# Optimization experiments

Hardware: AMD Instinct MI355X
Metric: run time of the kernel (lower is better)

## Reference

```python
import jax, jax.numpy as jnp
import numpy as np

N, IN_F, OUT_F = 8192, 4096, 4096
QMIN, QMAX = -128, 127  # int8 range for bitwidth 8


def setup_inputs() -> dict:
    key = jax.random.key(0)
    k1, k2, k3, k4 = jax.random.split(key, 4)
    x = jax.random.randint(k1, (N, IN_F), QMIN, QMAX + 1, dtype=jnp.int32).astype(jnp.int8)
    weight = jax.random.randint(k2, (OUT_F, IN_F), QMIN, QMAX + 1, dtype=jnp.int32).astype(jnp.int8)
    bias = jax.random.randint(k3, (OUT_F,), -1024, 1024, dtype=jnp.int32)
    weight_scale = jax.random.uniform(k4, (OUT_F,), dtype=jnp.float32, minval=0.001, maxval=0.02)
    input_scale = jnp.asarray([0.05], dtype=jnp.float32)
    output_scale = jnp.asarray([0.1], dtype=jnp.float32)
    output_zero_point = 0
    return {"x": x, "weight": weight, "bias": bias, "weight_scale": weight_scale,
            "input_scale": input_scale, "output_scale": output_scale,
            "output_zero_point": output_zero_point}


def reference(x, weight, bias, weight_scale, input_scale, output_scale, output_zero_point):
    # int32-accumulated GEMM with bias (CPU path of the torch module)
    acc = jnp.matmul(x.astype(jnp.int32), weight.astype(jnp.int32).T) + bias[None, :]  # [N, OUT_F] int32
    # fused dequant/requant epilogue
    scale_factor = (input_scale * weight_scale / output_scale)[None, :]  # [1, OUT_F]
    out = acc.astype(jnp.float32) * scale_factor + output_zero_point
    out = jnp.clip(jnp.round(out), QMIN, QMAX).astype(jnp.int8)
    return out
```

## Files before the change

### kernel.cpp

```cpp
#include <hip/hip_runtime.h>
#include <stdint.h>


#define M_DIM 8192
#define N_DIM 4096
#define K_DIM 4096
#define BM 128
#define BN 128
#define BK 64

using i32x4 = __attribute__((ext_vector_type(4))) int;

typedef const __attribute__((address_space(1))) uint32_t* gptr_t;
typedef __attribute__((address_space(3))) uint32_t* lptr_t;

__device__ __forceinline__ void gload_lds16(const void* g, void* l) {
    __builtin_amdgcn_global_load_lds((gptr_t)g, (lptr_t)l, 16, 0, 0);
}

__device__ __forceinline__ int pack4(i32x4 v) {
    return (int)(((unsigned)v.x & 0xFFu) | (((unsigned)v.y & 0xFFu) << 8) |
                 (((unsigned)v.z & 0xFFu) << 16) | (((unsigned)v.w) << 24));
}

__global__ void pack_i8_kernel(const int* __restrict__ src, int8_t* __restrict__ dst, int n_elems) {
    int idx = blockIdx.x * blockDim.x + threadIdx.x;
    int stride = gridDim.x * blockDim.x;
    int n16 = n_elems >> 4;
    for (int i = idx; i < n16; i += stride) {
        const i32x4* s = (const i32x4*)(src + (size_t)i * 16);
        i32x4 v0 = s[0], v1 = s[1], v2 = s[2], v3 = s[3];
        i32x4 o;
        o.x = pack4(v0); o.y = pack4(v1); o.z = pack4(v2); o.w = pack4(v3);
        *(i32x4*)(dst + (size_t)i * 16) = o;
    }
}

template<bool PACKED>
__global__ void qgemm_kernel(const void* __restrict__ xp, const void* __restrict__ wp,
                             const int* __restrict__ bias, const float* __restrict__ wscale,
                             const float* __restrict__ iscale, const float* __restrict__ oscale,
                             const int* __restrict__ zp, int* __restrict__ out) {
    __shared__ int8_t As[BM][BK];
    __shared__ int8_t Bs[BN][BK];

    const int tid  = threadIdx.x;
    const int wave = tid >> 6;
    const int lane = tid & 63;

    int b = blockIdx.x;
    int s = (b & 7) * (gridDim.x >> 3) + (b >> 3);
    const int bcol = (s & 31) * BN;
    const int brow = (s >> 5) * BM;

    const int wr = wave >> 1;
    const int wc = wave & 1;

    i32x4 acc[4][4] = {};

    for (int kt = 0; kt < K_DIM; kt += BK) {
        if constexpr (PACKED) {
            const int8_t* x8 = (const int8_t*)xp;
            const int8_t* w8 = (const int8_t*)wp;
            #pragma unroll
            for (int i = 0; i < 2; i++) {
                int c = wave * 2 + i;
                int row = c * 16 + (lane >> 2);
                int colb = (lane & 3) * 16;
                gload_lds16(x8 + (size_t)(brow + row) * K_DIM + kt + colb, &As[c * 16][0]);
                gload_lds16(w8 + (size_t)(bcol + row) * K_DIM + kt + colb, &Bs[c * 16][0]);
            }
        } else {
            const int* x32 = (const int*)xp;
            const int* w32 = (const int*)wp;
            int row = tid >> 1;
            int h = tid & 1;
            const i32x4* sa = (const i32x4*)(x32 + (size_t)(brow + row) * K_DIM + kt + h * 32);
            const i32x4* sb = (const i32x4*)(w32 + (size_t)(bcol + row) * K_DIM + kt + h * 32);
            int pa[8], pb[8];
            #pragma unroll
            for (int j = 0; j < 8; j++) { pa[j] = pack4(sa[j]); pb[j] = pack4(sb[j]); }
            *(i32x4*)&As[row][h * 32]      = *(i32x4*)&pa[0];
            *(i32x4*)&As[row][h * 32 + 16] = *(i32x4*)&pa[4];
            *(i32x4*)&Bs[row][h * 32]      = *(i32x4*)&pb[0];
            *(i32x4*)&Bs[row][h * 32 + 16] = *(i32x4*)&pb[4];
        }
        __syncthreads();

        i32x4 a_frag[4], b_frag[4];
        #pragma unroll
        for (int m = 0; m < 4; m++)
            a_frag[m] = *(const i32x4*)&As[wr * 64 + m * 16 + (lane & 15)][(lane >> 4) * 16];
        #pragma unroll
        for (int n = 0; n < 4; n++)
            b_frag[n] = *(const i32x4*)&Bs[wc * 64 + n * 16 + (lane & 15)][(lane >> 4) * 16];

        #pragma unroll
        for (int m = 0; m < 4; m++)
            #pragma unroll
            for (int n = 0; n < 4; n++)
                acc[m][n] = __builtin_amdgcn_mfma_i32_16x16x64_i8(a_frag[m], b_frag[n], acc[m][n], 0, 0, 0);

        __syncthreads();
    }

    const float is_v = iscale[0];
    const float os_v = oscale[0];
    const float zpf = (float)zp[0];
    #pragma unroll
    for (int n = 0; n < 4; n++) {
        int col = bcol + wc * 64 + n * 16 + (lane & 15);
        float sf = (is_v * wscale[col]) / os_v;
        int bz = bias[col];
        #pragma unroll
        for (int m = 0; m < 4; m++) {
            int row0 = brow + wr * 64 + m * 16 + (lane >> 4) * 4;
            #pragma unroll
            for (int r = 0; r < 4; r++) {
                float v = (float)(acc[m][n][r] + bz) * sf + zpf;
                v = rintf(v);
                v = fminf(fmaxf(v, -128.0f), 127.0f);
                out[(size_t)(row0 + r) * N_DIM + col] = (int)v;
            }
        }
    }
}

extern "C" void kernel_launch(void* const* d_in, const int* in_sizes, int n_in,
                              void* d_out, int out_size, void* d_ws, size_t ws_size,
                              hipStream_t stream) {
    const int*   x32    = (const int*)d_in[0];
    const int*   w32    = (const int*)d_in[1];
    const int*   bias   = (const int*)d_in[2];
    const float* wscale = (const float*)d_in[3];
    const float* iscale = (const float*)d_in[4];
    const float* oscale = (const float*)d_in[5];
    const int*   zp     = (const int*)d_in[6];
    int* out = (int*)d_out;

    const size_t need = (size_t)M_DIM * K_DIM + (size_t)N_DIM * K_DIM;
    const int nblocks = (M_DIM / BM) * (N_DIM / BN);

    if (ws_size >= need) {
        int8_t* x8 = (int8_t*)d_ws;
        int8_t* w8 = x8 + (size_t)M_DIM * K_DIM;
        pack_i8_kernel<<<2048, 256, 0, stream>>>(x32, x8, M_DIM * K_DIM);
        pack_i8_kernel<<<1024, 256, 0, stream>>>(w32, w8, N_DIM * K_DIM);
        qgemm_kernel<true><<<nblocks, 256, 0, stream>>>(x8, w8, bias, wscale, iscale, oscale, zp, out);
    } else {
        qgemm_kernel<false><<<nblocks, 256, 0, stream>>>(x32, w32, bias, wscale, iscale, oscale, zp, out);
    }
}
```

Baseline: 224.1 us.

## Add triple-buffered swizzled LDS pipeline with 128x256 tiles for int8 GEMM

Replaces the single-buffered packed GEMM with a 512-thread kernel using 128x256 tiles, BK of 128, and three LDS stages filled via asynchronous global-to-LDS loads. Each K step is split into four phases that interleave prefetch loads with MFMA groups, and uses XOR swizzling to avoid LDS bank conflicts plus s_setprio around the MFMAs. The aim is to hide global latency and raise data reuse per byte loaded. It needs 144KB of dynamic LDS, which limits the kernel to one block per CU, and it relies on hand-placed waitcnt and barriers.

```diff
diff --git a/kernel.cpp b/kernel.cpp
--- a/kernel.cpp
+++ b/kernel.cpp
@@ -6,8 +6,12 @@
 #define N_DIM 4096
 #define K_DIM 4096
 #define BM 128
-#define BN 128
-#define BK 64
+#define BN 256
+#define BKB 128
+#define NT (K_DIM / BKB)
+#define NBLK ((M_DIM / BM) * (N_DIM / BN))
+#define ABUF (BM * BKB)
+#define BBUF (BN * BKB)
 
 using i32x4 = __attribute__((ext_vector_type(4))) int;
 
@@ -36,57 +40,179 @@
     }
 }
 
-template<bool PACKED>
-__global__ void qgemm_kernel(const void* __restrict__ xp, const void* __restrict__ wp,
-                             const int* __restrict__ bias, const float* __restrict__ wscale,
-                             const float* __restrict__ iscale, const float* __restrict__ oscale,
-                             const int* __restrict__ zp, int* __restrict__ out) {
-    __shared__ int8_t As[BM][BK];
-    __shared__ int8_t Bs[BN][BK];
+#define MFMA_I8(a, b, c) __builtin_amdgcn_mfma_i32_16x16x64_i8((a), (b), (c), 0, 0, 0)
+
+#define RDA(m2, ks) (*(const i32x4*)(Acur + ((size_t)((qm)*32 + (m2)*16 + fr)) * BKB + ((((ks)*64 + fcol)) ^ fswz)))
+#define RDB(n2, ks) (*(const i32x4*)(Bcur + ((size_t)((qn)*32 + (n2)*16 + fr)) * BKB + ((((ks)*64 + fcol)) ^ fswz)))
+
+#define PHASE(qm_, qn_, STAGE_STMTS, TAIL_STMTS)                                  \
+  { constexpr int qm = (qm_); constexpr int qn = (qn_);                           \
+    i32x4 a00 = RDA(0,0), a01 = RDA(0,1), a10 = RDA(1,0), a11 = RDA(1,1);         \
+    i32x4 b00 = RDB(0,0), b01 = RDB(0,1), b10 = RDB(1,0), b11 = RDB(1,1);         \
+    STAGE_STMTS;                                                                  \
+    __builtin_amdgcn_s_barrier();                                                 \
+    asm volatile("s_waitcnt lgkmcnt(0)" ::: "memory");                            \
+    __builtin_amdgcn_sched_barrier(0);                                            \
+    __builtin_amdgcn_s_setprio(1);                                                \
+    acc[qm*2+0][qn*2+0] = MFMA_I8(a00, b00, acc[qm*2+0][qn*2+0]);                 \
+    acc[qm*2+0][qn*2+1] = MFMA_I8(a00, b10, acc[qm*2+0][qn*2+1]);                 \
+    acc[qm*2+1][qn*2+0] = MFMA_I8(a10, b00, acc[qm*2+1][qn*2+0]);                 \
+    acc[qm*2+1][qn*2+1] = MFMA_I8(a10, b10, acc[qm*2+1][qn*2+1]);                 \
+    acc[qm*2+0][qn*2+0] = MFMA_I8(a01, b01, acc[qm*2+0][qn*2+0]);                 \
+    acc[qm*2+0][qn*2+1] = MFMA_I8(a01, b11, acc[qm*2+0][qn*2+1]);                 \
+    acc[qm*2+1][qn*2+0] = MFMA_I8(a11, b01, acc[qm*2+1][qn*2+0]);                 \
+    acc[qm*2+1][qn*2+1] = MFMA_I8(a11, b11, acc[qm*2+1][qn*2+1]);                 \
+    __builtin_amdgcn_s_setprio(0);                                                \
+    TAIL_STMTS;                                                                   \
+    __builtin_amdgcn_s_barrier();                                                 \
+  }
+
+__global__ __launch_bounds__(512, 2)
+void qgemm8_kernel(const int8_t* __restrict__ x8, const int8_t* __restrict__ w8,
+                   const int* __restrict__ bias, const float* __restrict__ wscale,
+                   const float* __restrict__ iscale, const float* __restrict__ oscale,
+                   const int* __restrict__ zp, int* __restrict__ out) {
+    extern __shared__ int8_t lds[];
+    int8_t* As = lds;
+    int8_t* Bs = lds + 3 * ABUF;
 
     const int tid  = threadIdx.x;
     const int wave = tid >> 6;
     const int lane = tid & 63;
 
     int b = blockIdx.x;
+    int s = (b & 7) * (NBLK >> 3) + (b >> 3);
+    const int bcol = (s & 15) * BN;
+    const int brow = (s >> 4) * BM;
+
+    const int wr = wave >> 2;
+    const int wc = wave & 3;
+
+    const int sr8 = lane >> 3;
+    const int scs = ((lane & 7) * 16) ^ (sr8 << 4);
+    const int8_t* Ag = x8 + (size_t)(brow + wave * 16 + sr8) * K_DIM + scs;
+    const int8_t* Bg = w8 + (size_t)(bcol + wave * 32 + sr8) * K_DIM + scs;
+    const int aoff = wave * 2048;
+    const int boff = wave * 4096;
+
+    const int fr   = lane & 15;
+    const int fcol = (lane >> 4) * 16;
+    const int fswz = (lane & 7) << 4;
+
+    i32x4 acc[4][4] = {};
+
+    #pragma unroll
+    for (int t0 = 0; t0 < 2; t0++) {
+        int8_t* Ad = As + t0 * ABUF;
+        int8_t* Bd = Bs + t0 * BBUF;
+        const int8_t* Ak = Ag + (size_t)t0 * BKB;
+        const int8_t* Bk = Bg + (size_t)t0 * BKB;
+        gload_lds16(Ak,              Ad + aoff);
+        gload_lds16(Ak + 8 * K_DIM,  Ad + aoff + 1024);
+        gload_lds16(Bk,              Bd + boff);
+        gload_lds16(Bk + 8 * K_DIM,  Bd + boff + 1024);
+        gload_lds16(Bk + 16 * K_DIM, Bd + boff + 2048);
+        gload_lds16(Bk + 24 * K_DIM, Bd + boff + 3072);
+    }
+    asm volatile("s_waitcnt vmcnt(6)" ::: "memory");
+    __builtin_amdgcn_s_barrier();
+
+    int cur = 0, stg = 2;
+    for (int t = 0; t < NT - 2; ++t) {
+        const int8_t* Acur = As + cur * ABUF + (size_t)(wr * 64) * BKB;
+        const int8_t* Bcur = Bs + cur * BBUF + (size_t)(wc * 64) * BKB;
+        int8_t* Astg = As + stg * ABUF;
+        int8_t* Bstg = Bs + stg * BBUF;
+        const int8_t* AgK = Ag + (size_t)(t + 2) * BKB;
+        const int8_t* BgK = Bg + (size_t)(t + 2) * BKB;
+
+        PHASE(0, 0,
+              { gload_lds16(AgK,             Astg + aoff);
+                gload_lds16(BgK,             Bstg + boff); },
+              ((void)0))
+        PHASE(0, 1,
+              { gload_lds16(AgK + 8 * K_DIM, Astg + aoff + 1024);
+                gload_lds16(BgK + 8 * K_DIM, Bstg + boff + 1024); },
+              ((void)0))
+        PHASE(1, 0,
+              { gload_lds16(BgK + 16 * K_DIM, Bstg + boff + 2048); },
+              ((void)0))
+        PHASE(1, 1,
+              { gload_lds16(BgK + 24 * K_DIM, Bstg + boff + 3072); },
+              asm volatile("s_waitcnt vmcnt(6)" ::: "memory"))
+
+        cur = (cur == 2) ? 0 : cur + 1;
+        stg = (stg == 2) ? 0 : stg + 1;
+    }
+    {
+        const int8_t* Acur = As + cur * ABUF + (size_t)(wr * 64) * BKB;
+        const int8_t* Bcur = Bs + cur * BBUF + (size_t)(wc * 64) * BKB;
+        PHASE(0, 0, ((void)0), ((void)0))
+        PHASE(0, 1, ((void)0), ((void)0))
+        PHASE(1, 0, ((void)0), ((void)0))
+        PHASE(1, 1, ((void)0), asm volatile("s_waitcnt vmcnt(0)" ::: "memory"))
+        cur = (cur == 2) ? 0 : cur + 1;
+    }
+    {
+        const int8_t* Acur = As + cur * ABUF + (size_t)(wr * 64) * BKB;
+        const int8_t* Bcur = Bs + cur * BBUF + (size_t)(wc * 64) * BKB;
+        PHASE(0, 0, ((void)0), ((void)0))
+        PHASE(0, 1, ((void)0), ((void)0))
+        PHASE(1, 0, ((void)0), ((void)0))
+        PHASE(1, 1, ((void)0), ((void)0))
+    }
+
+    const float is_v = iscale[0];
+    const float os_v = oscale[0];
+    const float zpf = (float)zp[0];
+    #pragma unroll
+    for (int n = 0; n < 4; n++) {
+        int col = bcol + wc * 64 + n * 16 + (lane & 15);
+        float sf = (is_v * wscale[col]) / os_v;
+        int bz = bias[col];
+        #pragma unroll
+        for (int m = 0; m < 4; m++) {
+            int row0 = brow + wr * 64 + m * 16 + (lane >> 4) * 4;
+            #pragma unroll
+            for (int r = 0; r < 4; r++) {
+                float v = (float)(acc[m][n][r] + bz) * sf + zpf;
+                v = rintf(v);
+                v = fminf(fmaxf(v, -128.0f), 127.0f);
+                out[(size_t)(row0 + r) * N_DIM + col] = (int)v;
+            }
+        }
+    }
+}
+
+__global__ void qgemm_fallback(const int* __restrict__ x32, const int* __restrict__ w32,
+                               const int* __restrict__ bias, const float* __restrict__ wscale,
+                               const float* __restrict__ iscale, const float* __restrict__ oscale,
+                               const int* __restrict__ zp, int* __restrict__ out) {
+    __shared__ int8_t As[128][64];
+    __shared__ int8_t Bs[128][64];
+    const int tid  = threadIdx.x;
+    const int wave = tid >> 6;
+    const int lane = tid & 63;
+    int b = blockIdx.x;
     int s = (b & 7) * (gridDim.x >> 3) + (b >> 3);
-    const int bcol = (s & 31) * BN;
-    const int brow = (s >> 5) * BM;
-
+    const int bcol = (s & 31) * 128;
+    const int brow = (s >> 5) * 128;
     const int wr = wave >> 1;
     const int wc = wave & 1;
-
     i32x4 acc[4][4] = {};
-
-    for (int kt = 0; kt < K_DIM; kt += BK) {
-        if constexpr (PACKED) {
-            const int8_t* x8 = (const int8_t*)xp;
-            const int8_t* w8 = (const int8_t*)wp;
-            #pragma unroll
-            for (int i = 0; i < 2; i++) {
-                int c = wave * 2 + i;
-                int row = c * 16 + (lane >> 2);
-                int colb = (lane & 3) * 16;
-                gload_lds16(x8 + (size_t)(brow + row) * K_DIM + kt + colb, &As[c * 16][0]);
-                gload_lds16(w8 + (size_t)(bcol + row) * K_DIM + kt + colb, &Bs[c * 16][0]);
-            }
-        } else {
-            const int* x32 = (const int*)xp;
-            const int* w32 = (const int*)wp;
-            int row = tid >> 1;
-            int h = tid & 1;
-            const i32x4* sa = (const i32x4*)(x32 + (size_t)(brow + row) * K_DIM + kt + h * 32);
-            const i32x4* sb = (const i32x4*)(w32 + (size_t)(bcol + row) * K_DIM + kt + h * 32);
-            int pa[8], pb[8];
-            #pragma unroll
-            for (int j = 0; j < 8; j++) { pa[j] = pack4(sa[j]); pb[j] = pack4(sb[j]); }
-            *(i32x4*)&As[row][h * 32]      = *(i32x4*)&pa[0];
-            *(i32x4*)&As[row][h * 32 + 16] = *(i32x4*)&pa[4];
-            *(i32x4*)&Bs[row][h * 32]      = *(i32x4*)&pb[0];
-            *(i32x4*)&Bs[row][h * 32 + 16] = *(i32x4*)&pb[4];
-        }
+    for (int kt = 0; kt < K_DIM; kt += 64) {
+        int row = tid >> 1;
+        int h = tid & 1;
+        const i32x4* sa = (const i32x4*)(x32 + (size_t)(brow + row) * K_DIM + kt + h * 32);
+        const i32x4* sb = (const i32x4*)(w32 + (size_t)(bcol + row) * K_DIM + kt + h * 32);
+        int pa[8], pb[8];
+        #pragma unroll
+        for (int j = 0; j < 8; j++) { pa[j] = pack4(sa[j]); pb[j] = pack4(sb[j]); }
+        *(i32x4*)&As[row][h * 32]      = *(i32x4*)&pa[0];
+        *(i32x4*)&As[row][h * 32 + 16] = *(i32x4*)&pa[4];
+        *(i32x4*)&Bs[row][h * 32]      = *(i32x4*)&pb[0];
+        *(i32x4*)&Bs[row][h * 32 + 16] = *(i32x4*)&pb[4];
         __syncthreads();
-
         i32x4 a_frag[4], b_frag[4];
         #pragma unroll
         for (int m = 0; m < 4; m++)
@@ -94,16 +220,13 @@
         #pragma unroll
         for (int n = 0; n < 4; n++)
             b_frag[n] = *(const i32x4*)&Bs[wc * 64 + n * 16 + (lane & 15)][(lane >> 4) * 16];
-
         #pragma unroll
         for (int m = 0; m < 4; m++)
             #pragma unroll
             for (int n = 0; n < 4; n++)
-                acc[m][n] = __builtin_amdgcn_mfma_i32_16x16x64_i8(a_frag[m], b_frag[n], acc[m][n], 0, 0, 0);
-
+                acc[m][n] = MFMA_I8(a_frag[m], b_frag[n], acc[m][n]);
         __syncthreads();
     }
-
     const float is_v = iscale[0];
     const float os_v = oscale[0];
     const float zpf = (float)zp[0];
@@ -139,15 +262,18 @@
     int* out = (int*)d_out;
 
     const size_t need = (size_t)M_DIM * K_DIM + (size_t)N_DIM * K_DIM;
-    const int nblocks = (M_DIM / BM) * (N_DIM / BN);
+    const size_t lds_bytes = 3 * (size_t)(ABUF + BBUF);
 
     if (ws_size >= need) {
         int8_t* x8 = (int8_t*)d_ws;
         int8_t* w8 = x8 + (size_t)M_DIM * K_DIM;
         pack_i8_kernel<<<2048, 256, 0, stream>>>(x32, x8, M_DIM * K_DIM);
         pack_i8_kernel<<<1024, 256, 0, stream>>>(w32, w8, N_DIM * K_DIM);
-        qgemm_kernel<true><<<nblocks, 256, 0, stream>>>(x8, w8, bias, wscale, iscale, oscale, zp, out);
+        (void)hipFuncSetAttribute((const void*)qgemm8_kernel,
+                                  hipFuncAttributeMaxDynamicSharedMemorySize,
+                                  (int)lds_bytes);
+        qgemm8_kernel<<<NBLK, 512, lds_bytes, stream>>>(x8, w8, bias, wscale, iscale, oscale, zp, out);
     } else {
-        qgemm_kernel<false><<<nblocks, 256, 0, stream>>>(x32, w32, bias, wscale, iscale, oscale, zp, out);
-    }
-}
+        qgemm_fallback<<<2048, 256, 0, stream>>>(x32, w32, bias, wscale, iscale, oscale, zp, out);
+    }
+}
```

Result: no change. 220.5 us (-1.6%).
